# Kernel tuning notes

Hardware: AMD Instinct MI355X
Metric: run time of the kernel (lower is better)

The kernel has to match this reference:

```python
import jax, jax.numpy as jnp
import numpy as np

DIM = 2048
N_HEADS = 16
N_KV_HEADS = 8
HEAD_DIM = DIM // N_HEADS  # 128
N_REP = N_HEADS // N_KV_HEADS  # 2
HIDDEN = 4 * DIM  # Project hidden dim
SEQ = 2048
BSZ = 2
ROPE_THETA = 10000.0
NEG_INF = -1e9


def setup_inputs() -> dict:
    key = jax.random.key(0)
    ks = jax.random.split(key, 10)
    s_in = 1.0 / np.sqrt(DIM)
    s_hid = 1.0 / np.sqrt(HIDDEN)
    x = jax.random.normal(ks[0], (BSZ, SEQ, DIM), jnp.float32)
    wq = jax.random.normal(ks[1], (DIM, N_HEADS * HEAD_DIM), jnp.float32) * s_in
    wk_w1 = jax.random.normal(ks[2], (DIM, HIDDEN), jnp.float32) * s_in
    wk_w2 = jax.random.normal(ks[3], (HIDDEN, N_KV_HEADS * HEAD_DIM), jnp.float32) * s_hid
    wk_w3 = jax.random.normal(ks[4], (DIM, HIDDEN), jnp.float32) * s_in
    wv_w1 = jax.random.normal(ks[5], (DIM, HIDDEN), jnp.float32) * s_in
    wv_w2 = jax.random.normal(ks[6], (HIDDEN, N_KV_HEADS * HEAD_DIM), jnp.float32) * s_hid
    wv_w3 = jax.random.normal(ks[7], (DIM, HIDDEN), jnp.float32) * s_in
    wo = jax.random.normal(ks[8], (N_HEADS * HEAD_DIM, DIM), jnp.float32) * s_in
    # RoPE tables: angle[t, j] = t * theta^(-2j/head_dim), j in [0, head_dim/2)
    inv_freq = 1.0 / (ROPE_THETA ** (np.arange(0, HEAD_DIM, 2, dtype=np.float64) / HEAD_DIM))
    ang = np.outer(np.arange(SEQ, dtype=np.float64), inv_freq)
    freqs_cos = jnp.asarray(np.cos(ang), jnp.float32)  # [SEQ, HEAD_DIM//2]
    freqs_sin = jnp.asarray(np.sin(ang), jnp.float32)
    # causal additive mask [1, 1, SEQ, SEQ]
    mask = jnp.triu(jnp.full((SEQ, SEQ), NEG_INF, jnp.float32), k=1)[None, None]
    return {
        "x": x, "wq": wq,
        "wk_w1": wk_w1, "wk_w2": wk_w2, "wk_w3": wk_w3,
        "wv_w1": wv_w1, "wv_w2": wv_w2, "wv_w3": wv_w3,
        "wo": wo, "freqs_cos": freqs_cos, "freqs_sin": freqs_sin,
        "mask": mask, "start_pos": 0,
    }


def _rope(x, cos, sin):
    # x: [b, s, h, d]; pairs (x[2j], x[2j+1]) rotated as complex multiply
    xr = x[..., 0::2]
    xi = x[..., 1::2]
    c = cos[None, :, None, :]
    s = sin[None, :, None, :]
    out_r = xr * c - xi * s
    out_i = xr * s + xi * c
    return jnp.stack([out_r, out_i], axis=-1).reshape(x.shape)


def _project(x, w1, w2, w3):
    # SwiGLU-style projection: w2(silu(x@w1) * (x@w3))
    return (jax.nn.silu(x @ w1) * (x @ w3)) @ w2


def reference(x, wq, wk_w1, wk_w2, wk_w3, wv_w1, wv_w2, wv_w3, wo,
              freqs_cos, freqs_sin, mask, start_pos):
    b, s, _ = x.shape
    q = (x @ wq).reshape(b, s, N_HEADS, HEAD_DIM)
    q = _rope(q, freqs_cos, freqs_sin)
    k = _project(x, wk_w1, wk_w2, wk_w3).reshape(b, s, N_KV_HEADS, HEAD_DIM)
    v = _project(x, wv_w1, wv_w2, wv_w3).reshape(b, s, N_KV_HEADS, HEAD_DIM)
    k = _rope(k, freqs_cos, freqs_sin)
    o_keys, o_values = k, v  # is_training=True path: cache is just current k/v
    # repeat_kv (GQA) -> [b, h, s, d]
    kr = jnp.repeat(k, N_REP, axis=2).transpose(0, 2, 1, 3)
    vr = jnp.repeat(v, N_REP, axis=2).transpose(0, 2, 1, 3)
    qt = q.transpose(0, 2, 1, 3)
    scores = jnp.einsum('bhqd,bhkd->bhqk', qt, kr) / np.sqrt(HEAD_DIM).astype(np.float32)
    scores = scores + mask
    attn = jax.nn.softmax(scores.astype(jnp.float32), axis=-1).astype(qt.dtype)
    out = jnp.einsum('bhqk,bhkd->bhqd', attn, vr)
    out = out.transpose(0, 2, 1, 3).reshape(b, s, N_HEADS * HEAD_DIM)
    return (out @ wo, o_keys, o_values)
```

## Files before the change

kernel.cpp:

```cpp
#include <hip/hip_runtime.h>

typedef unsigned short ushort_t;
typedef __attribute__((ext_vector_type(4))) float f32x4;
typedef __attribute__((ext_vector_type(8))) __bf16 bf16x8;
typedef __attribute__((ext_vector_type(4))) unsigned short ushort4_t;
typedef __attribute__((ext_vector_type(8))) unsigned short ushort8_t;
typedef __attribute__((ext_vector_type(2))) unsigned int u32x2;

#define AS1 __attribute__((address_space(1)))
#define AS3 __attribute__((address_space(3)))

__device__ __forceinline__ float bf2f(ushort_t u) {
  unsigned int v = ((unsigned int)u) << 16;
  return __builtin_bit_cast(float, v);
}
__device__ __forceinline__ ushort_t f2bf(float f) {
  unsigned int u = __builtin_bit_cast(unsigned int, f);
  u += 0x7fffu + ((u >> 16) & 1u);
  return (ushort_t)(u >> 16);
}
__device__ __forceinline__ void storeC(float* p, float v) { *p = v; }
__device__ __forceinline__ void storeC(ushort_t* p, float v) { *p = f2bf(v); }

__global__ __launch_bounds__(256) void cast_f32_bf16(const float* __restrict__ in,
                                                     ushort_t* __restrict__ outp) {
  size_t i = ((size_t)blockIdx.x * 256 + threadIdx.x) * 4;
  f32x4 v = *(const f32x4*)(const void*)&in[i];
  ushort4_t o;
#pragma unroll
  for (int j = 0; j < 4; ++j) o[j] = f2bf(v[j]);
  *(ushort4_t*)(void*)&outp[i] = o;
}

__global__ __launch_bounds__(256) void transpose_cast_b(
    const float* __restrict__ W0, const float* __restrict__ W1,
    const float* __restrict__ W2, const float* __restrict__ W3,
    ushort_t* __restrict__ Wt, int K, int N, long long strT) {
  __shared__ float tile[32][33];
  const int z = blockIdx.z;
  const float* W = (z == 0) ? W0 : (z == 1) ? W1 : (z == 2) ? W2 : W3;
  ushort_t* out = Wt + (size_t)(strT * z);
  int n0 = blockIdx.x * 32, k0 = blockIdx.y * 32;
  int tx = threadIdx.x, ty = threadIdx.y;
#pragma unroll
  for (int i = 0; i < 4; ++i)
    tile[ty + 8 * i][tx] = W[(size_t)(k0 + ty + 8 * i) * N + n0 + tx];
  __syncthreads();
#pragma unroll
  for (int i = 0; i < 4; ++i)
    out[(size_t)(n0 + ty + 8 * i) * K + k0 + tx] = f2bf(tile[tx][ty + 8 * i]);
}

__global__ __launch_bounds__(256) void silu_mul(ushort_t* __restrict__ h1,
                                                const ushort_t* __restrict__ h3) {
  size_t i = ((size_t)blockIdx.x * 256 + threadIdx.x) * 8;
  ushort8_t a = *(const ushort8_t*)(const void*)&h1[i];
  ushort8_t b = *(const ushort8_t*)(const void*)&h3[i];
#pragma unroll
  for (int j = 0; j < 8; ++j) {
    float x = bf2f(a[j]);
    float g = x / (1.0f + __expf(-x));
    a[j] = f2bf(g * bf2f(b[j]));
  }
  *(ushort8_t*)(void*)&h1[i] = a;
}

__global__ __launch_bounds__(256) void reduce_q(const ushort_t* __restrict__ part,
                                                ushort_t* __restrict__ qb,
                                                const float* __restrict__ fc,
                                                const float* __restrict__ fs) {
  const float alpha = 0.08838834764831845f;
  int p = blockIdx.x * 256 + threadIdx.x;
  size_t e0 = (size_t)p * 8;
  int i0 = (int)((e0 & 127) >> 1);
  int s = (int)((e0 >> 11) & 2047);
  ushort8_t a = *(const ushort8_t*)(const void*)&part[e0];
  ushort8_t b = *(const ushort8_t*)(const void*)&part[e0 + 8388608];
  f32x4 c4 = *(const f32x4*)(const void*)&fc[s * 64 + i0];
  f32x4 s4 = *(const f32x4*)(const void*)&fs[s * 64 + i0];
  ushort8_t o;
#pragma unroll
  for (int j = 0; j < 4; ++j) {
    float xr = bf2f(a[2 * j]) + bf2f(b[2 * j]);
    float xi = bf2f(a[2 * j + 1]) + bf2f(b[2 * j + 1]);
    float c = c4[j] * alpha, sn = s4[j] * alpha;
    o[2 * j] = f2bf(xr * c - xi * sn);
    o[2 * j + 1] = f2bf(xr * sn + xi * c);
  }
  *(ushort8_t*)(void*)&qb[e0] = o;
}

__global__ __launch_bounds__(256) void reduce_k(const ushort_t* __restrict__ part,
                                                ushort_t* __restrict__ kb,
                                                float* __restrict__ okeys,
                                                const float* __restrict__ fc,
                                                const float* __restrict__ fs) {
  int p = blockIdx.x * 256 + threadIdx.x;
  size_t e0 = (size_t)p * 8;
  int i0 = (int)((e0 & 127) >> 1);
  int s = (int)((e0 >> 10) & 2047);
  ushort8_t a0 = *(const ushort8_t*)(const void*)&part[e0];
  ushort8_t a1 = *(const ushort8_t*)(const void*)&part[e0 + 4194304];
  ushort8_t a2 = *(const ushort8_t*)(const void*)&part[e0 + 8388608];
  ushort8_t a3 = *(const ushort8_t*)(const void*)&part[e0 + 12582912];
  f32x4 c4 = *(const f32x4*)(const void*)&fc[s * 64 + i0];
  f32x4 s4 = *(const f32x4*)(const void*)&fs[s * 64 + i0];
  ushort8_t o;
  f32x4 ov0, ov1;
#pragma unroll
  for (int j = 0; j < 4; ++j) {
    float xr = bf2f(a0[2 * j]) + bf2f(a1[2 * j]) + bf2f(a2[2 * j]) + bf2f(a3[2 * j]);
    float xi = bf2f(a0[2 * j + 1]) + bf2f(a1[2 * j + 1]) + bf2f(a2[2 * j + 1]) +
               bf2f(a3[2 * j + 1]);
    float c = c4[j], sn = s4[j];
    float orr = xr * c - xi * sn;
    float oi = xr * sn + xi * c;
    o[2 * j] = f2bf(orr);
    o[2 * j + 1] = f2bf(oi);
    if (j < 2) { ov0[2 * j] = orr; ov0[2 * j + 1] = oi; }
    else       { ov1[2 * (j - 2)] = orr; ov1[2 * (j - 2) + 1] = oi; }
  }
  *(ushort8_t*)(void*)&kb[e0] = o;
  *(f32x4*)(void*)&okeys[e0] = ov0;
  *(f32x4*)(void*)&okeys[e0 + 4] = ov1;
}

__global__ __launch_bounds__(256) void reduce_v(const ushort_t* __restrict__ part,
                                                float* __restrict__ ovals,
                                                ushort_t* __restrict__ vbT) {
  __shared__ ushort_t tile[32][33];
  int s0 = blockIdx.x * 32, d0 = blockIdx.y * 32, bk = blockIdx.z;
  int b = bk >> 3, kh = bk & 7;
  int tx = threadIdx.x, ty = threadIdx.y;
#pragma unroll
  for (int i = 0; i < 4; ++i) {
    int s = s0 + ty + 8 * i;
    size_t src = ((size_t)(b * 2048 + s)) * 1024 + kh * 128 + d0 + tx;
    float v = bf2f(part[src]) + bf2f(part[src + 4194304]) +
              bf2f(part[src + 8388608]) + bf2f(part[src + 12582912]);
    tile[ty + 8 * i][tx] = f2bf(v);
    ovals[src] = v;
  }
  __syncthreads();
#pragma unroll
  for (int i = 0; i < 4; ++i) {
    int d = d0 + ty + 8 * i;
    vbT[((size_t)bk * 128 + d) * 2048 + s0 + tx] = tile[tx][ty + 8 * i];
  }
}

__global__ __launch_bounds__(256) void reduce_wo(const float* __restrict__ part,
                                                 float* __restrict__ outp) {
  size_t i = ((size_t)blockIdx.x * 256 + threadIdx.x) * 4;
  f32x4 a = *(const f32x4*)(const void*)&part[i];
  f32x4 b = *(const f32x4*)(const void*)&part[i + 8388608];
  *(f32x4*)(void*)&outp[i] = a + b;
}

__global__ __launch_bounds__(256) void flash_attn(
    const ushort_t* __restrict__ Q, const ushort_t* __restrict__ Kg,
    const ushort_t* __restrict__ VT, ushort_t* __restrict__ O) {
  __shared__ __align__(16) char smem[81920];
  const int xp = blockIdx.x;
  const int bh = blockIdx.y;
  const int b = bh >> 4, h = bh & 15, kh = h >> 1;
  const int t = threadIdx.x, w = t >> 6, lane = t & 63;
  const int fr = lane & 15, fh = lane >> 4;
  const size_t kelem0 = ((size_t)b * 2048) * 1024 + kh * 128;
  const size_t velem0 = ((size_t)(b * 8 + kh)) * 128 * 2048;
  const size_t qrow0 = (size_t)b * 2048;

  size_t oK[4], oV[4];
#pragma unroll
  for (int qv = 0; qv < 4; ++qv) {
    int row = w * 16 + qv * 4 + (lane >> 4);
    oK[qv] = (size_t)row * 1024 + (((lane & 15) ^ (row & 7)) * 8);
    int rd = w * 32 + qv * 8 + (lane >> 3);
    oV[qv] = (size_t)rd * 2048 + (((lane & 7) ^ (rd & 7)) * 8);
  }

  auto stage = [&](int tile, int buf) {
    const size_t kc = (size_t)tile * 64 * 1024;
    const int vc = tile * 64;
    char* kd = smem + buf * 16384 + w * 4096;
    char* vd = smem + 32768 + buf * 16384 + w * 4096;
#pragma unroll
    for (int qv = 0; qv < 4; ++qv) {
      __builtin_amdgcn_global_load_lds((const AS1 void*)(Kg + kelem0 + kc + oK[qv]),
                                       (AS3 void*)(kd + qv * 1024), 16, 0, 0);
      __builtin_amdgcn_global_load_lds((const AS1 void*)(VT + velem0 + oV[qv] + vc),
                                       (AS3 void*)(vd + qv * 1024), 16, 0, 0);
    }
  };

#pragma unroll 1
  for (int ph = 0; ph < 2; ++ph) {
    const int qi = ph ? (15 - xp) : xp;
    const int qw = qi * 128 + w * 32;
    const int nt = 2 * qi + 2;

    bf16x8 qF[2][4];
#pragma unroll
    for (int qt = 0; qt < 2; ++qt)
#pragma unroll
      for (int i = 0; i < 4; ++i)
        qF[qt][i] = *(const bf16x8*)(const void*)(
            Q + (qrow0 + qw + qt * 16 + fr) * 2048 + h * 128 + i * 32 + fh * 8);

    f32x4 acco[8][2] = {};
    float mrun[2] = {-1e30f, -1e30f};
    float lrun[2] = {0.0f, 0.0f};

    stage(0, 0);
#pragma unroll 1
    for (int tt = 0; tt < nt; ++tt) {
      const int c0 = tt * 64;
      if (tt + 1 < nt) {
        stage(tt + 1, (tt + 1) & 1);
        asm volatile("s_waitcnt vmcnt(8)" ::: "memory");
      } else {
        asm volatile("s_waitcnt vmcnt(0)" ::: "memory");
      }
      __builtin_amdgcn_sched_barrier(0);
      __builtin_amdgcn_s_barrier();
      const char* KL = smem + (tt & 1) * 16384;
      const char* VL = smem + 32768 + (tt & 1) * 16384;
      char* PL = smem + 65536 + w * 4096;
      if (c0 <= qw + 31) {
        f32x4 sacc[2][4] = {};
#pragma unroll
        for (int i = 0; i < 4; ++i)
#pragma unroll
          for (int mt = 0; mt < 4; ++mt) {
            bf16x8 kf = *(const bf16x8*)(const void*)(
                KL + (mt * 16 + fr) * 256 + (((i * 4 + fh) ^ (fr & 7)) * 16));
            sacc[0][mt] = __builtin_amdgcn_mfma_f32_16x16x32_bf16(kf, qF[0][i], sacc[0][mt], 0, 0, 0);
            sacc[1][mt] = __builtin_amdgcn_mfma_f32_16x16x32_bf16(kf, qF[1][i], sacc[1][mt], 0, 0, 0);
          }
        if (c0 + 63 > qw) {
#pragma unroll
          for (int qt = 0; qt < 2; ++qt) {
            int qg = qw + qt * 16 + fr;
#pragma unroll
            for (int mt = 0; mt < 4; ++mt)
#pragma unroll
              for (int j = 0; j < 4; ++j)
                if (c0 + mt * 16 + fh * 4 + j > qg) sacc[qt][mt][j] = -1e30f;
          }
        }
#pragma unroll
        for (int qt = 0; qt < 2; ++qt) {
          float mt_ = -1e30f;
#pragma unroll
          for (int mt = 0; mt < 4; ++mt)
#pragma unroll
            for (int j = 0; j < 4; ++j) mt_ = fmaxf(mt_, sacc[qt][mt][j]);
          mt_ = fmaxf(mt_, __shfl_xor(mt_, 16, 64));
          mt_ = fmaxf(mt_, __shfl_xor(mt_, 32, 64));
          float mnew = fmaxf(mrun[qt], mt_);
          float corr = __expf(mrun[qt] - mnew);
          mrun[qt] = mnew;
          float ps = 0.0f;
          float pv[4][4];
#pragma unroll
          for (int mt = 0; mt < 4; ++mt)
#pragma unroll
            for (int j = 0; j < 4; ++j) {
              float pe = __expf(sacc[qt][mt][j] - mnew);
              pv[mt][j] = pe;
              ps += pe;
            }
          ps += __shfl_xor(ps, 16, 64);
          ps += __shfl_xor(ps, 32, 64);
          lrun[qt] = lrun[qt] * corr + ps;
#pragma unroll
          for (int mt = 0; mt < 4; ++mt) {
            unsigned int u0, u1;
            asm("v_cvt_pk_bf16_f32 %0, %1, %2" : "=v"(u0) : "v"(pv[mt][0]), "v"(pv[mt][1]));
            asm("v_cvt_pk_bf16_f32 %0, %1, %2" : "=v"(u1) : "v"(pv[mt][2]), "v"(pv[mt][3]));
            u32x2 val;
            val[0] = u0;
            val[1] = u1;
            *(u32x2*)(void*)(PL + qt * 2048 + fr * 128 +
                             (((2 * mt + (fh >> 1)) ^ (fr & 7)) * 16) + (fh & 1) * 8) = val;
          }
#pragma unroll
          for (int dt = 0; dt < 8; ++dt) acco[dt][qt] *= corr;
        }
        bf16x8 pf[2][2];
#pragma unroll
        for (int qt = 0; qt < 2; ++qt)
#pragma unroll
          for (int ks = 0; ks < 2; ++ks)
            pf[qt][ks] = *(const bf16x8*)(const void*)(
                PL + qt * 2048 + fr * 128 + (((ks * 4 + fh) ^ (fr & 7)) * 16));
#pragma unroll
        for (int dt = 0; dt < 8; ++dt)
#pragma unroll
          for (int ks = 0; ks < 2; ++ks) {
            bf16x8 vf = *(const bf16x8*)(const void*)(
                VL + (dt * 16 + fr) * 128 + (((ks * 4 + fh) ^ (fr & 7)) * 16));
            acco[dt][0] = __builtin_amdgcn_mfma_f32_16x16x32_bf16(vf, pf[0][ks], acco[dt][0], 0, 0, 0);
            acco[dt][1] = __builtin_amdgcn_mfma_f32_16x16x32_bf16(vf, pf[1][ks], acco[dt][1], 0, 0, 0);
          }
      }
      __builtin_amdgcn_s_barrier();
    }
#pragma unroll
    for (int qt = 0; qt < 2; ++qt) {
      float inv = 1.0f / lrun[qt];
      const size_t rb = (qrow0 + qw + qt * 16 + fr) * 2048 + h * 128;
#pragma unroll
      for (int dt = 0; dt < 8; ++dt) {
        ushort4_t o4;
#pragma unroll
        for (int j = 0; j < 4; ++j) o4[j] = f2bf(acco[dt][qt][j] * inv);
        *(ushort4_t*)(void*)(O + rb + dt * 16 + fh * 4) = o4;
      }
    }
  }
}

template <typename CT>
__global__ __launch_bounds__(512, 4) void gemm256(
    const ushort_t* __restrict__ A, const ushort_t* __restrict__ B,
    CT* __restrict__ C, int K, int lda, int ldb, int ldc,
    int nwgx, int nwg, long long strA, long long strB, long long strC) {
  __shared__ __align__(16) char smem[49152];
  const int bz = blockIdx.y;
  const int bid = blockIdx.x;
  const int swz = (bid & 7) * (nwg >> 3) + (bid >> 3);
  const int r0 = (swz / nwgx) * 128;
  const int c0 = (swz % nwgx) * 256;
  const int t = threadIdx.x, w = t >> 6, lane = t & 63;
  const int wm = w >> 2, wn = w & 3;
  const int fr = lane & 15, fh = lane >> 4;
  const int sl2 = (fh ^ ((fr >> 1) & 3)) << 4;
  const int srow = t >> 2;
  const int scb = (t & 3) ^ ((srow >> 1) & 3);
  const int NT = K >> 5;
  const ushort_t* gA = A + strA * bz + (size_t)(r0 + srow) * lda + scb * 8;
  const ushort_t* gB = B + strB * bz + (size_t)(c0 + srow) * ldb + scb * 8;

  auto stage = [&](int tile) {
    const int buf = tile & 1;
    __builtin_amdgcn_global_load_lds(
        (const AS1 void*)(gA + tile * 32),
        (AS3 void*)((char*)smem + buf * 8192 + t * 16), 16, 0, 0);
    __builtin_amdgcn_global_load_lds(
        (const AS1 void*)(gB + tile * 32),
        (AS3 void*)((char*)smem + 16384 + buf * 16384 + t * 16), 16, 0, 0);
    __builtin_amdgcn_global_load_lds(
        (const AS1 void*)(gB + (size_t)128 * ldb + tile * 32),
        (AS3 void*)((char*)smem + 16384 + buf * 16384 + 8192 + t * 16), 16, 0, 0);
  };

  f32x4 acc[4][4] = {};

  stage(0);
  asm volatile("s_waitcnt vmcnt(0)" ::: "memory");
  __builtin_amdgcn_sched_barrier(0);
  __builtin_amdgcn_s_barrier();
  __builtin_amdgcn_sched_barrier(0);

  const int aBase = wm * 4096 + fr * 64 + sl2;
  const int bBase = 16384 + wn * 4096 + fr * 64 + sl2;

  for (int kt = 0; kt < NT; ++kt) {
    if (kt + 1 < NT) stage(kt + 1);
    const char* la = (const char*)smem + ((kt & 1) * 8192) + aBase;
    const char* lb = (const char*)smem + ((kt & 1) * 16384) + bBase;
    bf16x8 aF[4], bF[4];
#pragma unroll
    for (int m = 0; m < 4; ++m)
      aF[m] = *(const bf16x8*)(const void*)(la + m * 1024);
#pragma unroll
    for (int n = 0; n < 4; ++n)
      bF[n] = *(const bf16x8*)(const void*)(lb + n * 1024);
    __builtin_amdgcn_sched_barrier(0);
    __builtin_amdgcn_s_setprio(1);
#pragma unroll
    for (int m = 0; m < 4; ++m)
#pragma unroll
      for (int n = 0; n < 4; ++n)
        acc[m][n] = __builtin_amdgcn_mfma_f32_16x16x32_bf16(aF[m], bF[n], acc[m][n], 0, 0, 0);
    __builtin_amdgcn_s_setprio(0);
    if (kt + 1 < NT) {
      asm volatile("s_waitcnt vmcnt(0)" ::: "memory");
      __builtin_amdgcn_sched_barrier(0);
      __builtin_amdgcn_s_barrier();
      __builtin_amdgcn_sched_barrier(0);
    }
  }

  CT* gC = C + strC * bz;
  const int cr = r0 + wm * 64 + fh * 4;
  const int cc = c0 + wn * 64 + fr;
#pragma unroll
  for (int m = 0; m < 4; ++m)
#pragma unroll
    for (int n = 0; n < 4; ++n)
#pragma unroll
      for (int j = 0; j < 4; ++j)
        storeC(&gC[(size_t)(cr + m * 16 + j) * ldc + cc + n * 16], acc[m][n][j]);
}

extern "C" void kernel_launch(void* const* d_in, const int* in_sizes, int n_in,
                              void* d_out, int out_size, void* d_ws, size_t ws_size,
                              hipStream_t stream) {
  const float* x = (const float*)d_in[0];
  const float* wq = (const float*)d_in[1];
  const float* wk1 = (const float*)d_in[2];
  const float* wk2 = (const float*)d_in[3];
  const float* wk3 = (const float*)d_in[4];
  const float* wv1 = (const float*)d_in[5];
  const float* wv2 = (const float*)d_in[6];
  const float* wv3 = (const float*)d_in[7];
  const float* wo = (const float*)d_in[8];
  const float* fc = (const float*)d_in[9];
  const float* fs = (const float*)d_in[10];

  float* outp = (float*)d_out;
  float* okeys = outp + 8388608;
  float* ovals = outp + 12582912;

  char* p = (char*)d_ws;
  auto alloc = [&](size_t bytes) {
    char* r = p;
    p += (bytes + 255) & ~(size_t)255;
    return r;
  };
  ushort_t* xb = (ushort_t*)alloc(8388608ull * 2);
  ushort_t* w4T = (ushort_t*)alloc(4ull * 16777216 * 2);
  ushort_t* w2T = (ushort_t*)alloc(2ull * 8388608 * 2);
  ushort_t* wqoT = (ushort_t*)alloc(2ull * 4194304 * 2);
  ushort_t* qb = (ushort_t*)alloc(8388608ull * 2);
  ushort_t* kb = (ushort_t*)alloc(4194304ull * 2);
  ushort_t* vbT = (ushort_t*)alloc(4194304ull * 2);
  ushort_t* ob = (ushort_t*)alloc(8388608ull * 2);
  char* hreg = alloc(134217728ull);
  ushort_t* h1 = (ushort_t*)hreg;
  ushort_t* partQ16 = (ushort_t*)hreg;
  float* partWO = (float*)hreg;
  ushort_t* part16 = (ushort_t*)w4T;

  ushort_t* wk1T = w4T;
  ushort_t* wk2T = w2T;
  ushort_t* wv1T = w4T + 2ull * 16777216;
  ushort_t* wv2T = w2T + 8388608;
  ushort_t* wqT = wqoT;
  ushort_t* woT = wqoT + 4194304;

  dim3 tb(32, 8);

  cast_f32_bf16<<<8192, 256, 0, stream>>>(x, xb);
  transpose_cast_b<<<dim3(256, 64, 4), tb, 0, stream>>>(wk1, wk3, wv1, wv3, w4T,
                                                        2048, 8192, 16777216);
  transpose_cast_b<<<dim3(32, 256, 2), tb, 0, stream>>>(wk2, wv2, wk2, wv2, w2T,
                                                        8192, 1024, 8388608);
  transpose_cast_b<<<dim3(64, 64, 2), tb, 0, stream>>>(wq, wo, wq, wo, wqoT,
                                                       2048, 2048, 4194304);

  gemm256<ushort_t><<<dim3(256, 2), 512, 0, stream>>>(
      xb, wqT, partQ16, 1024, 2048, 2048, 2048, 8, 256, 1024, 1024, 8388608);
  reduce_q<<<4096, 256, 0, stream>>>(partQ16, qb, fc, fs);

  gemm256<ushort_t><<<dim3(1024, 2), 512, 0, stream>>>(
      xb, wk1T, h1, 2048, 2048, 2048, 8192, 32, 1024, 0, 16777216, 33554432);
  silu_mul<<<16384, 256, 0, stream>>>(h1, h1 + 33554432);
  gemm256<ushort_t><<<dim3(128, 4), 512, 0, stream>>>(
      h1, wk2T, part16, 2048, 8192, 8192, 1024, 4, 128, 2048, 2048, 4194304);
  reduce_k<<<2048, 256, 0, stream>>>(part16, kb, okeys, fc, fs);

  gemm256<ushort_t><<<dim3(1024, 2), 512, 0, stream>>>(
      xb, wv1T, h1, 2048, 2048, 2048, 8192, 32, 1024, 0, 16777216, 33554432);
  silu_mul<<<16384, 256, 0, stream>>>(h1, h1 + 33554432);
  gemm256<ushort_t><<<dim3(128, 4), 512, 0, stream>>>(
      h1, wv2T, part16, 2048, 8192, 8192, 1024, 4, 128, 2048, 2048, 4194304);
  reduce_v<<<dim3(64, 4, 16), tb, 0, stream>>>(part16, ovals, vbT);

  flash_attn<<<dim3(8, 32), 256, 0, stream>>>(qb, kb, vbT, ob);

  gemm256<float><<<dim3(256, 2), 512, 0, stream>>>(
      ob, woT, partWO, 1024, 2048, 2048, 2048, 8, 256, 1024, 1024, 8388608);
  reduce_wo<<<8192, 256, 0, stream>>>(partWO, outp);

  (void)in_sizes; (void)n_in; (void)out_size; (void)ws_size;
}
```

Before: 1.091 ms.

## Enlarge GEMM tiles, fuse SwiGLU into GEMM epilogue, split flash-attn per block

The GEMM is rebuilt around 256x256 tiles with a 64-wide K step, a deeper double-buffered LDS pipeline and 128KB of shared memory, with occupancy lowered to two blocks. The W1/W3 weights are interleaved during the transpose so a new GLU GEMM computes both projections in one pass and applies SiLU*mul in its epilogue, which removes the separate silu_mul kernel and its traffic over the hidden activations. Flash attention now launches one q-tile per block with a mirrored mapping instead of two phases per block. The Wo split-K partials are stored in bf16 rather than fp32, which halves that traffic but adds rounding error to the final output.

```diff
diff --git a/kernel.cpp b/kernel.cpp
--- a/kernel.cpp
+++ b/kernel.cpp
@@ -51,18 +51,27 @@
     out[(size_t)(n0 + ty + 8 * i) * K + k0 + tx] = f2bf(tile[tx][ty + 8 * i]);
 }
 
-__global__ __launch_bounds__(256) void silu_mul(ushort_t* __restrict__ h1,
-                                                const ushort_t* __restrict__ h3) {
-  size_t i = ((size_t)blockIdx.x * 256 + threadIdx.x) * 8;
-  ushort8_t a = *(const ushort8_t*)(const void*)&h1[i];
-  ushort8_t b = *(const ushort8_t*)(const void*)&h3[i];
-#pragma unroll
-  for (int j = 0; j < 8; ++j) {
-    float x = bf2f(a[j]);
-    float g = x / (1.0f + __expf(-x));
-    a[j] = f2bf(g * bf2f(b[j]));
-  }
-  *(ushort8_t*)(void*)&h1[i] = a;
+__global__ __launch_bounds__(256) void transpose_cast_glu(
+    const float* __restrict__ W1k, const float* __restrict__ W3k,
+    const float* __restrict__ W1v, const float* __restrict__ W3v,
+    ushort_t* __restrict__ out, long long strT) {
+  __shared__ float tile[32][33];
+  const int z = blockIdx.z;
+  const float* W = (z == 0) ? W1k : (z == 1) ? W3k : (z == 2) ? W1v : W3v;
+  ushort_t* o = out + (size_t)((z >> 1) * strT);
+  const int zz = z & 1;
+  int n0 = blockIdx.x * 32, k0 = blockIdx.y * 32;
+  int tx = threadIdx.x, ty = threadIdx.y;
+#pragma unroll
+  for (int i = 0; i < 4; ++i)
+    tile[ty + 8 * i][tx] = W[(size_t)(k0 + ty + 8 * i) * 8192 + n0 + tx];
+  __syncthreads();
+#pragma unroll
+  for (int i = 0; i < 4; ++i) {
+    int n = n0 + ty + 8 * i;
+    int br = ((n >> 4) * 32) + zz * 16 + (n & 15);
+    o[(size_t)br * 2048 + k0 + tx] = f2bf(tile[tx][ty + 8 * i]);
+  }
 }
 
 __global__ __launch_bounds__(256) void reduce_q(const ushort_t* __restrict__ part,
@@ -149,20 +158,28 @@
   }
 }
 
-__global__ __launch_bounds__(256) void reduce_wo(const float* __restrict__ part,
+__global__ __launch_bounds__(256) void reduce_wo(const ushort_t* __restrict__ part,
                                                  float* __restrict__ outp) {
-  size_t i = ((size_t)blockIdx.x * 256 + threadIdx.x) * 4;
-  f32x4 a = *(const f32x4*)(const void*)&part[i];
-  f32x4 b = *(const f32x4*)(const void*)&part[i + 8388608];
-  *(f32x4*)(void*)&outp[i] = a + b;
+  size_t e0 = ((size_t)blockIdx.x * 256 + threadIdx.x) * 8;
+  ushort8_t a = *(const ushort8_t*)(const void*)&part[e0];
+  ushort8_t b = *(const ushort8_t*)(const void*)&part[e0 + 8388608];
+  f32x4 o0, o1;
+#pragma unroll
+  for (int j = 0; j < 4; ++j) {
+    o0[j] = bf2f(a[j]) + bf2f(b[j]);
+    o1[j] = bf2f(a[j + 4]) + bf2f(b[j + 4]);
+  }
+  *(f32x4*)(void*)&outp[e0] = o0;
+  *(f32x4*)(void*)&outp[e0 + 4] = o1;
 }
 
 __global__ __launch_bounds__(256) void flash_attn(
     const ushort_t* __restrict__ Q, const ushort_t* __restrict__ Kg,
     const ushort_t* __restrict__ VT, ushort_t* __restrict__ O) {
   __shared__ __align__(16) char smem[81920];
-  const int xp = blockIdx.x;
+  const int xq = blockIdx.x;
   const int bh = blockIdx.y;
+  const int qi = (bh & 16) ? (15 - xq) : xq;
   const int b = bh >> 4, h = bh & 15, kh = h >> 1;
   const int t = threadIdx.x, w = t >> 6, lane = t & 63;
   const int fr = lane & 15, fh = lane >> 4;
@@ -193,216 +210,283 @@
     }
   };
 
+  const int qw = qi * 128 + w * 32;
+  const int nt = 2 * qi + 2;
+
+  bf16x8 qF[2][4];
+#pragma unroll
+  for (int qt = 0; qt < 2; ++qt)
+#pragma unroll
+    for (int i = 0; i < 4; ++i)
+      qF[qt][i] = *(const bf16x8*)(const void*)(
+          Q + (qrow0 + qw + qt * 16 + fr) * 2048 + h * 128 + i * 32 + fh * 8);
+
+  f32x4 acco[8][2] = {};
+  float mrun[2] = {-1e30f, -1e30f};
+  float lrun[2] = {0.0f, 0.0f};
+
+  stage(0, 0);
 #pragma unroll 1
-  for (int ph = 0; ph < 2; ++ph) {
-    const int qi = ph ? (15 - xp) : xp;
-    const int qw = qi * 128 + w * 32;
-    const int nt = 2 * qi + 2;
-
-    bf16x8 qF[2][4];
-#pragma unroll
-    for (int qt = 0; qt < 2; ++qt)
+  for (int tt = 0; tt < nt; ++tt) {
+    const int c0 = tt * 64;
+    if (tt + 1 < nt) {
+      stage(tt + 1, (tt + 1) & 1);
+      asm volatile("s_waitcnt vmcnt(8)" ::: "memory");
+    } else {
+      asm volatile("s_waitcnt vmcnt(0)" ::: "memory");
+    }
+    __builtin_amdgcn_sched_barrier(0);
+    __builtin_amdgcn_s_barrier();
+    const char* KL = smem + (tt & 1) * 16384;
+    const char* VL = smem + 32768 + (tt & 1) * 16384;
+    char* PL = smem + 65536 + w * 4096;
+    if (c0 <= qw + 31) {
+      f32x4 sacc[2][4] = {};
 #pragma unroll
       for (int i = 0; i < 4; ++i)
-        qF[qt][i] = *(const bf16x8*)(const void*)(
-            Q + (qrow0 + qw + qt * 16 + fr) * 2048 + h * 128 + i * 32 + fh * 8);
-
-    f32x4 acco[8][2] = {};
-    float mrun[2] = {-1e30f, -1e30f};
-    float lrun[2] = {0.0f, 0.0f};
-
-    stage(0, 0);
-#pragma unroll 1
-    for (int tt = 0; tt < nt; ++tt) {
-      const int c0 = tt * 64;
-      if (tt + 1 < nt) {
-        stage(tt + 1, (tt + 1) & 1);
-        asm volatile("s_waitcnt vmcnt(8)" ::: "memory");
-      } else {
-        asm volatile("s_waitcnt vmcnt(0)" ::: "memory");
+#pragma unroll
+        for (int mt = 0; mt < 4; ++mt) {
+          bf16x8 kf = *(const bf16x8*)(const void*)(
+              KL + (mt * 16 + fr) * 256 + (((i * 4 + fh) ^ (fr & 7)) * 16));
+          sacc[0][mt] = __builtin_amdgcn_mfma_f32_16x16x32_bf16(kf, qF[0][i], sacc[0][mt], 0, 0, 0);
+          sacc[1][mt] = __builtin_amdgcn_mfma_f32_16x16x32_bf16(kf, qF[1][i], sacc[1][mt], 0, 0, 0);
+        }
+      if (c0 + 63 > qw) {
+#pragma unroll
+        for (int qt = 0; qt < 2; ++qt) {
+          int qg = qw + qt * 16 + fr;
+#pragma unroll
+          for (int mt = 0; mt < 4; ++mt)
+#pragma unroll
+            for (int j = 0; j < 4; ++j)
+              if (c0 + mt * 16 + fh * 4 + j > qg) sacc[qt][mt][j] = -1e30f;
+        }
       }
-      __builtin_amdgcn_sched_barrier(0);
-      __builtin_amdgcn_s_barrier();
-      const char* KL = smem + (tt & 1) * 16384;
-      const char* VL = smem + 32768 + (tt & 1) * 16384;
-      char* PL = smem + 65536 + w * 4096;
-      if (c0 <= qw + 31) {
-        f32x4 sacc[2][4] = {};
-#pragma unroll
-        for (int i = 0; i < 4; ++i)
-#pragma unroll
-          for (int mt = 0; mt < 4; ++mt) {
-            bf16x8 kf = *(const bf16x8*)(const void*)(
-                KL + (mt * 16 + fr) * 256 + (((i * 4 + fh) ^ (fr & 7)) * 16));
-            sacc[0][mt] = __builtin_amdgcn_mfma_f32_16x16x32_bf16(kf, qF[0][i], sacc[0][mt], 0, 0, 0);
-            sacc[1][mt] = __builtin_amdgcn_mfma_f32_16x16x32_bf16(kf, qF[1][i], sacc[1][mt], 0, 0, 0);
+#pragma unroll
+      for (int qt = 0; qt < 2; ++qt) {
+        float mt_ = -1e30f;
+#pragma unroll
+        for (int mt = 0; mt < 4; ++mt)
+#pragma unroll
+          for (int j = 0; j < 4; ++j) mt_ = fmaxf(mt_, sacc[qt][mt][j]);
+        mt_ = fmaxf(mt_, __shfl_xor(mt_, 16, 64));
+        mt_ = fmaxf(mt_, __shfl_xor(mt_, 32, 64));
+        float mnew = fmaxf(mrun[qt], mt_);
+        float corr = __expf(mrun[qt] - mnew);
+        mrun[qt] = mnew;
+        float ps = 0.0f;
+        float pv[4][4];
+#pragma unroll
+        for (int mt = 0; mt < 4; ++mt)
+#pragma unroll
+          for (int j = 0; j < 4; ++j) {
+            float pe = __expf(sacc[qt][mt][j] - mnew);
+            pv[mt][j] = pe;
+            ps += pe;
           }
-        if (c0 + 63 > qw) {
-#pragma unroll
-          for (int qt = 0; qt < 2; ++qt) {
-            int qg = qw + qt * 16 + fr;
-#pragma unroll
-            for (int mt = 0; mt < 4; ++mt)
-#pragma unroll
-              for (int j = 0; j < 4; ++j)
-                if (c0 + mt * 16 + fh * 4 + j > qg) sacc[qt][mt][j] = -1e30f;
-          }
+        ps += __shfl_xor(ps, 16, 64);
+        ps += __shfl_xor(ps, 32, 64);
+        lrun[qt] = lrun[qt] * corr + ps;
+#pragma unroll
+        for (int mt = 0; mt < 4; ++mt) {
+          unsigned int u0, u1;
+          asm("v_cvt_pk_bf16_f32 %0, %1, %2" : "=v"(u0) : "v"(pv[mt][0]), "v"(pv[mt][1]));
+          asm("v_cvt_pk_bf16_f32 %0, %1, %2" : "=v"(u1) : "v"(pv[mt][2]), "v"(pv[mt][3]));
+          u32x2 val;
+          val[0] = u0;
+          val[1] = u1;
+          *(u32x2*)(void*)(PL + qt * 2048 + fr * 128 +
+                           (((2 * mt + (fh >> 1)) ^ (fr & 7)) * 16) + (fh & 1) * 8) = val;
         }
 #pragma unroll
-        for (int qt = 0; qt < 2; ++qt) {
-          float mt_ = -1e30f;
-#pragma unroll
-          for (int mt = 0; mt < 4; ++mt)
-#pragma unroll
-            for (int j = 0; j < 4; ++j) mt_ = fmaxf(mt_, sacc[qt][mt][j]);
-          mt_ = fmaxf(mt_, __shfl_xor(mt_, 16, 64));
-          mt_ = fmaxf(mt_, __shfl_xor(mt_, 32, 64));
-          float mnew = fmaxf(mrun[qt], mt_);
-          float corr = __expf(mrun[qt] - mnew);
-          mrun[qt] = mnew;
-          float ps = 0.0f;
-          float pv[4][4];
-#pragma unroll
-          for (int mt = 0; mt < 4; ++mt)
-#pragma unroll
-            for (int j = 0; j < 4; ++j) {
-              float pe = __expf(sacc[qt][mt][j] - mnew);
-              pv[mt][j] = pe;
-              ps += pe;
-            }
-          ps += __shfl_xor(ps, 16, 64);
-          ps += __shfl_xor(ps, 32, 64);
-          lrun[qt] = lrun[qt] * corr + ps;
-#pragma unroll
-          for (int mt = 0; mt < 4; ++mt) {
-            unsigned int u0, u1;
-            asm("v_cvt_pk_bf16_f32 %0, %1, %2" : "=v"(u0) : "v"(pv[mt][0]), "v"(pv[mt][1]));
-            asm("v_cvt_pk_bf16_f32 %0, %1, %2" : "=v"(u1) : "v"(pv[mt][2]), "v"(pv[mt][3]));
-            u32x2 val;
-            val[0] = u0;
-            val[1] = u1;
-            *(u32x2*)(void*)(PL + qt * 2048 + fr * 128 +
-                             (((2 * mt + (fh >> 1)) ^ (fr & 7)) * 16) + (fh & 1) * 8) = val;
-          }
-#pragma unroll
-          for (int dt = 0; dt < 8; ++dt) acco[dt][qt] *= corr;
+        for (int dt = 0; dt < 8; ++dt) acco[dt][qt] *= corr;
+      }
+      bf16x8 pf[2][2];
+#pragma unroll
+      for (int qt = 0; qt < 2; ++qt)
+#pragma unroll
+        for (int ks = 0; ks < 2; ++ks)
+          pf[qt][ks] = *(const bf16x8*)(const void*)(
+              PL + qt * 2048 + fr * 128 + (((ks * 4 + fh) ^ (fr & 7)) * 16));
+#pragma unroll
+      for (int dt = 0; dt < 8; ++dt)
+#pragma unroll
+        for (int ks = 0; ks < 2; ++ks) {
+          bf16x8 vf = *(const bf16x8*)(const void*)(
+              VL + (dt * 16 + fr) * 128 + (((ks * 4 + fh) ^ (fr & 7)) * 16));
+          acco[dt][0] = __builtin_amdgcn_mfma_f32_16x16x32_bf16(vf, pf[0][ks], acco[dt][0], 0, 0, 0);
+          acco[dt][1] = __builtin_amdgcn_mfma_f32_16x16x32_bf16(vf, pf[1][ks], acco[dt][1], 0, 0, 0);
         }
-        bf16x8 pf[2][2];
-#pragma unroll
-        for (int qt = 0; qt < 2; ++qt)
-#pragma unroll
-          for (int ks = 0; ks < 2; ++ks)
-            pf[qt][ks] = *(const bf16x8*)(const void*)(
-                PL + qt * 2048 + fr * 128 + (((ks * 4 + fh) ^ (fr & 7)) * 16));
-#pragma unroll
-        for (int dt = 0; dt < 8; ++dt)
-#pragma unroll
-          for (int ks = 0; ks < 2; ++ks) {
-            bf16x8 vf = *(const bf16x8*)(const void*)(
-                VL + (dt * 16 + fr) * 128 + (((ks * 4 + fh) ^ (fr & 7)) * 16));
-            acco[dt][0] = __builtin_amdgcn_mfma_f32_16x16x32_bf16(vf, pf[0][ks], acco[dt][0], 0, 0, 0);
-            acco[dt][1] = __builtin_amdgcn_mfma_f32_16x16x32_bf16(vf, pf[1][ks], acco[dt][1], 0, 0, 0);
-          }
-      }
-      __builtin_amdgcn_s_barrier();
     }
-#pragma unroll
-    for (int qt = 0; qt < 2; ++qt) {
-      float inv = 1.0f / lrun[qt];
-      const size_t rb = (qrow0 + qw + qt * 16 + fr) * 2048 + h * 128;
-#pragma unroll
-      for (int dt = 0; dt < 8; ++dt) {
-        ushort4_t o4;
-#pragma unroll
-        for (int j = 0; j < 4; ++j) o4[j] = f2bf(acco[dt][qt][j] * inv);
-        *(ushort4_t*)(void*)(O + rb + dt * 16 + fh * 4) = o4;
-      }
+    __builtin_amdgcn_s_barrier();
+  }
+#pragma unroll
+  for (int qt = 0; qt < 2; ++qt) {
+    float inv = 1.0f / lrun[qt];
+    const size_t rb = (qrow0 + qw + qt * 16 + fr) * 2048 + h * 128;
+#pragma unroll
+    for (int dt = 0; dt < 8; ++dt) {
+      ushort4_t o4;
+#pragma unroll
+      for (int j = 0; j < 4; ++j) o4[j] = f2bf(acco[dt][qt][j] * inv);
+      *(ushort4_t*)(void*)(O + rb + dt * 16 + fh * 4) = o4;
     }
   }
 }
 
+#define GEMM_PHASE(ABUF, BBUF, Q, STAGE_STMT, TAIL_STMT)                        \
+  {                                                                             \
+    if ((Q) == 0) {                                                             \
+      _Pragma("unroll") for (int nf = 0; nf < 4; ++nf) {                        \
+        const char* bp = (BBUF) + ((wn * 64 + nf * 16 + fr) << 7);              \
+        bF[nf][0] = *(const bf16x8*)(const void*)(bp + sl);                     \
+        bF[nf][1] = *(const bf16x8*)(const void*)(bp + (sl ^ 64));              \
+      }                                                                         \
+    }                                                                           \
+    _Pragma("unroll") for (int mi = 0; mi < 2; ++mi) {                          \
+      const char* ap = (ABUF) + ((wm * 128 + ((Q)*2 + mi) * 16 + fr) << 7);     \
+      aF[mi][0] = *(const bf16x8*)(const void*)(ap + sl);                       \
+      aF[mi][1] = *(const bf16x8*)(const void*)(ap + (sl ^ 64));                \
+    }                                                                           \
+    STAGE_STMT;                                                                 \
+    if ((Q) == 0) asm volatile("s_waitcnt lgkmcnt(8)" ::: "memory");            \
+    __builtin_amdgcn_s_barrier();                                               \
+    asm volatile("s_waitcnt lgkmcnt(0)" ::: "memory");                          \
+    __builtin_amdgcn_sched_barrier(0);                                          \
+    __builtin_amdgcn_s_setprio(1);                                              \
+    _Pragma("unroll") for (int mi = 0; mi < 2; ++mi)                            \
+      _Pragma("unroll") for (int nf = 0; nf < 4; ++nf) {                        \
+        acc[(Q)*2 + mi][nf] = __builtin_amdgcn_mfma_f32_16x16x32_bf16(          \
+            aF[mi][0], bF[nf][0], acc[(Q)*2 + mi][nf], 0, 0, 0);                \
+        acc[(Q)*2 + mi][nf] = __builtin_amdgcn_mfma_f32_16x16x32_bf16(          \
+            aF[mi][1], bF[nf][1], acc[(Q)*2 + mi][nf], 0, 0, 0);                \
+      }                                                                         \
+    __builtin_amdgcn_s_setprio(0);                                              \
+    TAIL_STMT;                                                                  \
+    __builtin_amdgcn_sched_barrier(0);                                          \
+    __builtin_amdgcn_s_barrier();                                               \
+  }
+
+#define GEMM_BODY                                                               \
+  f32x4 acc[8][4] = {};                                                         \
+  const int NT = K >> 6;                                                        \
+  const int NI = NT >> 1;                                                       \
+  char* const A0 = (char*)smem;                                                 \
+  char* const A1 = (char*)smem + 32768;                                         \
+  char* const B0 = (char*)smem + 65536;                                         \
+  char* const B1 = (char*)smem + 98304;                                         \
+         \
+  auto stageA = [&](int tile, int h) {                                          \
+    char* base = (char*)smem + ((tile & 1) << 15);                              \
+    const ushort_t* src = gA + tile * 64 + (size_t)(h * 64) * lda;              \
+    __builtin_amdgcn_global_load_lds((const AS1 void*)src,                      \
+        (AS3 void*)(base + h * 8192 + w * 1024), 16, 0, 0);                     \
+    __builtin_amdgcn_global_load_lds(                                           \
+        (const AS1 void*)(src + (size_t)128 * lda),                             \
+        (AS3 void*)(base + 16384 + h * 8192 + w * 1024), 16, 0, 0);             \
+  };                                                                            \
+  auto stageB = [&](int tile, int h) {                                          \
+    char* base = (char*)smem + 65536 + ((tile & 1) << 15);                      \
+    const ushort_t* src = gB + tile * 64 + (size_t)(h * 128) * ldb;             \
+    __builtin_amdgcn_global_load_lds((const AS1 void*)src,                      \
+        (AS3 void*)(base + h * 16384 + w * 1024), 16, 0, 0);                    \
+    __builtin_amdgcn_global_load_lds(                                           \
+        (const AS1 void*)(src + (size_t)64 * ldb),                              \
+        (AS3 void*)(base + h * 16384 + 8192 + w * 1024), 16, 0, 0);             \
+  };                                                                            \
+     \
+  stageB(0, 0); stageB(0, 1); stageA(0, 0); stageA(0, 1);                       \
+  stageB(1, 0); stageB(1, 1); stageA(1, 0);                                     \
+  asm volatile("s_waitcnt vmcnt(6)" ::: "memory");                              \
+  __builtin_amdgcn_sched_barrier(0);                                            \
+  __builtin_amdgcn_s_barrier();                                                 \
+  __builtin_amdgcn_sched_barrier(0);                                            \
+  for (int i = 0; i < NI; ++i) {                                                \
+    const int T1 = 2 * i + 1, T2 = 2 * i + 2, T3 = 2 * i + 3;                   \
+    const bool s2 = T2 < NT, s3 = T3 < NT;                                      \
+    bf16x8 bF[4][2], aF[2][2];                                                  \
+                                            \
+    GEMM_PHASE(A0, B0, 0, { stageA(T1, 1); }, {})                               \
+    GEMM_PHASE(A0, B0, 1, { if (s2) stageB(T2, 0); }, {})                       \
+    GEMM_PHASE(A0, B0, 2, { if (s2) stageB(T2, 1); }, {})                       \
+    GEMM_PHASE(A0, B0, 3, { if (s2) stageA(T2, 0); },                           \
+               { if (s2) asm volatile("s_waitcnt vmcnt(6)" ::: "memory");       \
+                 else    asm volatile("s_waitcnt vmcnt(0)" ::: "memory"); })    \
+                                          \
+    GEMM_PHASE(A1, B1, 0, { if (s2) stageA(T2, 1); }, {})                       \
+    GEMM_PHASE(A1, B1, 1, { if (s3) stageB(T3, 0); }, {})                       \
+    GEMM_PHASE(A1, B1, 2, { if (s3) stageB(T3, 1); }, {})                       \
+    GEMM_PHASE(A1, B1, 3, { if (s3) stageA(T3, 0); },                           \
+               { if (s2) asm volatile("s_waitcnt vmcnt(6)" ::: "memory"); })    \
+  }
+
 template <typename CT>
-__global__ __launch_bounds__(512, 4) void gemm256(
+__global__ __launch_bounds__(512, 2) void gemm256(
     const ushort_t* __restrict__ A, const ushort_t* __restrict__ B,
     CT* __restrict__ C, int K, int lda, int ldb, int ldc,
     int nwgx, int nwg, long long strA, long long strB, long long strC) {
-  __shared__ __align__(16) char smem[49152];
+  __shared__ __align__(16) char smem[131072];
   const int bz = blockIdx.y;
   const int bid = blockIdx.x;
   const int swz = (bid & 7) * (nwg >> 3) + (bid >> 3);
-  const int r0 = (swz / nwgx) * 128;
+  const int r0 = (swz / nwgx) * 256;
   const int c0 = (swz % nwgx) * 256;
   const int t = threadIdx.x, w = t >> 6, lane = t & 63;
   const int wm = w >> 2, wn = w & 3;
   const int fr = lane & 15, fh = lane >> 4;
-  const int sl2 = (fh ^ ((fr >> 1) & 3)) << 4;
-  const int srow = t >> 2;
-  const int scb = (t & 3) ^ ((srow >> 1) & 3);
-  const int NT = K >> 5;
+  const int sl = (fh ^ (fr & 7)) << 4;
+  const int srow = t >> 3;
+  const int scb = (t & 7) ^ (srow & 7);
   const ushort_t* gA = A + strA * bz + (size_t)(r0 + srow) * lda + scb * 8;
   const ushort_t* gB = B + strB * bz + (size_t)(c0 + srow) * ldb + scb * 8;
 
-  auto stage = [&](int tile) {
-    const int buf = tile & 1;
-    __builtin_amdgcn_global_load_lds(
-        (const AS1 void*)(gA + tile * 32),
-        (AS3 void*)((char*)smem + buf * 8192 + t * 16), 16, 0, 0);
-    __builtin_amdgcn_global_load_lds(
-        (const AS1 void*)(gB + tile * 32),
-        (AS3 void*)((char*)smem + 16384 + buf * 16384 + t * 16), 16, 0, 0);
-    __builtin_amdgcn_global_load_lds(
-        (const AS1 void*)(gB + (size_t)128 * ldb + tile * 32),
-        (AS3 void*)((char*)smem + 16384 + buf * 16384 + 8192 + t * 16), 16, 0, 0);
-  };
-
-  f32x4 acc[4][4] = {};
-
-  stage(0);
-  asm volatile("s_waitcnt vmcnt(0)" ::: "memory");
-  __builtin_amdgcn_sched_barrier(0);
-  __builtin_amdgcn_s_barrier();
-  __builtin_amdgcn_sched_barrier(0);
-
-  const int aBase = wm * 4096 + fr * 64 + sl2;
-  const int bBase = 16384 + wn * 4096 + fr * 64 + sl2;
-
-  for (int kt = 0; kt < NT; ++kt) {
-    if (kt + 1 < NT) stage(kt + 1);
-    const char* la = (const char*)smem + ((kt & 1) * 8192) + aBase;
-    const char* lb = (const char*)smem + ((kt & 1) * 16384) + bBase;
-    bf16x8 aF[4], bF[4];
-#pragma unroll
-    for (int m = 0; m < 4; ++m)
-      aF[m] = *(const bf16x8*)(const void*)(la + m * 1024);
-#pragma unroll
-    for (int n = 0; n < 4; ++n)
-      bF[n] = *(const bf16x8*)(const void*)(lb + n * 1024);
-    __builtin_amdgcn_sched_barrier(0);
-    __builtin_amdgcn_s_setprio(1);
-#pragma unroll
-    for (int m = 0; m < 4; ++m)
-#pragma unroll
-      for (int n = 0; n < 4; ++n)
-        acc[m][n] = __builtin_amdgcn_mfma_f32_16x16x32_bf16(aF[m], bF[n], acc[m][n], 0, 0, 0);
-    __builtin_amdgcn_s_setprio(0);
-    if (kt + 1 < NT) {
-      asm volatile("s_waitcnt vmcnt(0)" ::: "memory");
-      __builtin_amdgcn_sched_barrier(0);
-      __builtin_amdgcn_s_barrier();
-      __builtin_amdgcn_sched_barrier(0);
-    }
-  }
+  GEMM_BODY
 
   CT* gC = C + strC * bz;
-  const int cr = r0 + wm * 64 + fh * 4;
+  const int cr = r0 + wm * 128 + fh * 4;
   const int cc = c0 + wn * 64 + fr;
 #pragma unroll
-  for (int m = 0; m < 4; ++m)
+  for (int m = 0; m < 8; ++m)
 #pragma unroll
     for (int n = 0; n < 4; ++n)
 #pragma unroll
       for (int j = 0; j < 4; ++j)
         storeC(&gC[(size_t)(cr + m * 16 + j) * ldc + cc + n * 16], acc[m][n][j]);
+}
+
+__global__ __launch_bounds__(512, 2) void gemm256_glu(
+    const ushort_t* __restrict__ A, const ushort_t* __restrict__ B,
+    ushort_t* __restrict__ C, int K, int lda, int ldb, int ldc,
+    int nwgx, int nwg) {
+  __shared__ __align__(16) char smem[131072];
+  const int bid = blockIdx.x;
+  const int swz = (bid & 7) * (nwg >> 3) + (bid >> 3);
+  const int r0 = (swz / nwgx) * 256;
+  const int c0 = (swz % nwgx) * 256;
+  const int t = threadIdx.x, w = t >> 6, lane = t & 63;
+  const int wm = w >> 2, wn = w & 3;
+  const int fr = lane & 15, fh = lane >> 4;
+  const int sl = (fh ^ (fr & 7)) << 4;
+  const int srow = t >> 3;
+  const int scb = (t & 7) ^ (srow & 7);
+  const ushort_t* gA = A + (size_t)(r0 + srow) * lda + scb * 8;
+  const ushort_t* gB = B + (size_t)(c0 + srow) * ldb + scb * 8;
+
+  GEMM_BODY
+
+  const int cr = r0 + wm * 128 + fh * 4;
+  const int cc2 = (c0 >> 1) + wn * 32 + fr;
+#pragma unroll
+  for (int m = 0; m < 8; ++m)
+#pragma unroll
+    for (int pp = 0; pp < 2; ++pp)
+#pragma unroll
+      for (int j = 0; j < 4; ++j) {
+        float g1 = acc[m][2 * pp][j];
+        float g3 = acc[m][2 * pp + 1][j];
+        float hv = g1 / (1.0f + __expf(-g1)) * g3;
+        C[(size_t)(cr + m * 16 + j) * ldc + cc2 + pp * 16] = f2bf(hv);
+      }
 }
 
 extern "C" void kernel_launch(void* const* d_in, const int* in_sizes, int n_in,
@@ -439,14 +523,14 @@
   ushort_t* vbT = (ushort_t*)alloc(4194304ull * 2);
   ushort_t* ob = (ushort_t*)alloc(8388608ull * 2);
   char* hreg = alloc(134217728ull);
-  ushort_t* h1 = (ushort_t*)hreg;
+  ushort_t* hbuf = (ushort_t*)hreg;
   ushort_t* partQ16 = (ushort_t*)hreg;
-  float* partWO = (float*)hreg;
+  ushort_t* partWO16 = (ushort_t*)hreg;
   ushort_t* part16 = (ushort_t*)w4T;
 
-  ushort_t* wk1T = w4T;
+  ushort_t* Bk = w4T;
+  ushort_t* Bv = w4T + 2ull * 16777216;
   ushort_t* wk2T = w2T;
-  ushort_t* wv1T = w4T + 2ull * 16777216;
   ushort_t* wv2T = w2T + 8388608;
   ushort_t* wqT = wqoT;
   ushort_t* woT = wqoT + 4194304;
@@ -454,36 +538,34 @@
   dim3 tb(32, 8);
 
   cast_f32_bf16<<<8192, 256, 0, stream>>>(x, xb);
-  transpose_cast_b<<<dim3(256, 64, 4), tb, 0, stream>>>(wk1, wk3, wv1, wv3, w4T,
-                                                        2048, 8192, 16777216);
+  transpose_cast_glu<<<dim3(256, 64, 4), tb, 0, stream>>>(wk1, wk3, wv1, wv3,
+                                                          w4T, 33554432);
   transpose_cast_b<<<dim3(32, 256, 2), tb, 0, stream>>>(wk2, wv2, wk2, wv2, w2T,
                                                         8192, 1024, 8388608);
   transpose_cast_b<<<dim3(64, 64, 2), tb, 0, stream>>>(wq, wo, wq, wo, wqoT,
                                                        2048, 2048, 4194304);
 
-  gemm256<ushort_t><<<dim3(256, 2), 512, 0, stream>>>(
-      xb, wqT, partQ16, 1024, 2048, 2048, 2048, 8, 256, 1024, 1024, 8388608);
+  gemm256<ushort_t><<<dim3(128, 2), 512, 0, stream>>>(
+      xb, wqT, partQ16, 1024, 2048, 2048, 2048, 8, 128, 1024, 1024, 8388608);
   reduce_q<<<4096, 256, 0, stream>>>(partQ16, qb, fc, fs);
 
-  gemm256<ushort_t><<<dim3(1024, 2), 512, 0, stream>>>(
-      xb, wk1T, h1, 2048, 2048, 2048, 8192, 32, 1024, 0, 16777216, 33554432);
-  silu_mul<<<16384, 256, 0, stream>>>(h1, h1 + 33554432);
-  gemm256<ushort_t><<<dim3(128, 4), 512, 0, stream>>>(
-      h1, wk2T, part16, 2048, 8192, 8192, 1024, 4, 128, 2048, 2048, 4194304);
+  gemm256_glu<<<dim3(1024, 1), 512, 0, stream>>>(
+      xb, Bk, hbuf, 2048, 2048, 2048, 8192, 64, 1024);
+  gemm256<ushort_t><<<dim3(64, 4), 512, 0, stream>>>(
+      hbuf, wk2T, part16, 2048, 8192, 8192, 1024, 4, 64, 2048, 2048, 4194304);
   reduce_k<<<2048, 256, 0, stream>>>(part16, kb, okeys, fc, fs);
 
-  gemm256<ushort_t><<<dim3(1024, 2), 512, 0, stream>>>(
-      xb, wv1T, h1, 2048, 2048, 2048, 8192, 32, 1024, 0, 16777216, 33554432);
-  silu_mul<<<16384, 256, 0, stream>>>(h1, h1 + 33554432);
-  gemm256<ushort_t><<<dim3(128, 4), 512, 0, stream>>>(
-      h1, wv2T, part16, 2048, 8192, 8192, 1024, 4, 128, 2048, 2048, 4194304);
+  gemm256_glu<<<dim3(1024, 1), 512, 0, stream>>>(
+      xb, Bv, hbuf, 2048, 2048, 2048, 8192, 64, 1024);
+  gemm256<ushort_t><<<dim3(64, 4), 512, 0, stream>>>(
+      hbuf, wv2T, part16, 2048, 8192, 8192, 1024, 4, 64, 2048, 2048, 4194304);
   reduce_v<<<dim3(64, 4, 16), tb, 0, stream>>>(part16, ovals, vbT);
 
-  flash_attn<<<dim3(8, 32), 256, 0, stream>>>(qb, kb, vbT, ob);
-
-  gemm256<float><<<dim3(256, 2), 512, 0, stream>>>(
-      ob, woT, partWO, 1024, 2048, 2048, 2048, 8, 256, 1024, 1024, 8388608);
-  reduce_wo<<<8192, 256, 0, stream>>>(partWO, outp);
+  flash_attn<<<dim3(16, 32), 256, 0, stream>>>(qb, kb, vbT, ob);
+
+  gemm256<ushort_t><<<dim3(128, 2), 512, 0, stream>>>(
+      ob, woT, partWO16, 1024, 2048, 2048, 2048, 8, 128, 1024, 1024, 8388608);
+  reduce_wo<<<4096, 256, 0, stream>>>(partWO16, outp);
 
   (void)in_sizes; (void)n_in; (void)out_size; (void)ws_size;
 }
```

After: 933.7 us. -14.4%, faster.
